# Kernel tuning notes

Hardware: AMD Instinct MI355X
Metric: run time of the kernel (lower is better)

## Reference

```python
import jax, jax.numpy as jnp
import numpy as np

B, H, W, CIN = 4, 32, 32, 3
COUT, NPAR = 4, 16

# Ansatz3x3 gate list: (control, target, base param index); each entry applies
# CRZ(theta[k], control, target) then CRX(theta[k+1], control, target).
GATES = [(1, 0, 0), (3, 2, 2), (2, 0, 4), (8, 7, 6),
         (5, 4, 8), (7, 6, 10), (6, 4, 12), (4, 0, 14)]
NQ = 9


def setup_inputs() -> dict:
    key = jax.random.key(0)
    k1, k2 = jax.random.split(key)
    x = jax.random.uniform(k1, (B, H, W, CIN), dtype=jnp.float32)
    q_params = jax.random.uniform(k2, (COUT, NPAR), minval=-np.pi, maxval=np.pi,
                                  dtype=jnp.float32)
    return {"x": x, "q_params": q_params}


def _rz_mat(th):
    # RZ(th) = diag(e^{-i th/2}, e^{+i th/2}); th: [C] -> [C,2,2]
    e = jnp.exp(-0.5j * th.astype(jnp.complex64))
    z = jnp.zeros_like(e)
    return jnp.stack([jnp.stack([e, z], -1), jnp.stack([z, jnp.conj(e)], -1)], -2)


def _rx_mat(th):
    # RX(th) = [[cos, -i sin], [-i sin, cos]] with half-angle; th: [C] -> [C,2,2]
    c = jnp.cos(0.5 * th).astype(jnp.complex64)
    s = (-1j * jnp.sin(0.5 * th)).astype(jnp.complex64)
    return jnp.stack([jnp.stack([c, s], -1), jnp.stack([s, c], -1)], -2)


def _apply_ctrl(state, U, control, target):
    # state: [C, P] + [2]*NQ (axis 2+q is qubit q); U: [C,2,2] applied on target
    # when control qubit is 1.
    ax_c, ax_t = 2 + control, 2 + target
    s0, s1 = jnp.split(state, 2, axis=ax_c)
    s1 = jnp.moveaxis(s1, ax_t, -1)
    s1 = jnp.einsum('cab,c...b->c...a', U, s1)
    s1 = jnp.moveaxis(s1, -1, ax_t)
    return jnp.concatenate([s0, s1], axis=ax_c)


def _quanv_forward(x, q_params):
    cout = q_params.shape[0]
    b, h, w = x.shape[0], x.shape[1], x.shape[2]
    fx, fy = h - 2, w - 2  # stride 1
    avg = jnp.mean(x, axis=-1)  # [B,H,W]
    # 3x3 patches, row-major flatten matching .flatten(): [B,fx,fy,9]
    patches = jnp.stack([avg[:, i:i + fx, j:j + fy]
                         for i in range(3) for j in range(3)], axis=-1)
    angles = 2.0 * jnp.pi * patches - jnp.pi
    # RX(angle)|0> = [cos(a/2), -i sin(a/2)] per qubit -> product state
    a0 = jnp.cos(0.5 * angles).astype(jnp.complex64)
    a1 = (-1j * jnp.sin(0.5 * angles)).astype(jnp.complex64)
    amps = jnp.stack([a0, a1], axis=-1).reshape(b * fx * fy, NQ, 2)  # [P,9,2]
    P = b * fx * fy
    state = amps[:, 0, :]  # [P,2]
    for q in range(1, NQ):
        state = state[..., None] * amps[:, q, :].reshape((P,) + (1,) * q + (2,))
    # replicate over output channels (params differ per channel)
    state = jnp.broadcast_to(state[None], (cout,) + state.shape) + 0j  # [C,P,2,...,2]
    for (ctrl, tgt, k) in GATES:
        state = _apply_ctrl(state, _rz_mat(q_params[:, k]), ctrl, tgt)
        state = _apply_ctrl(state, _rx_mat(q_params[:, k + 1]), ctrl, tgt)
    # avgZ = (p0 - p1 + 1)/2 = P(qubit0 = 0); qubit 0 is axis 2
    s = state[:, :, 0]  # [C,P] + [2]*8
    p0 = jnp.sum(s.real ** 2 + s.imag ** 2, axis=tuple(range(2, 2 + NQ - 1)))  # [C,P]
    out = jnp.zeros((b, h, w, cout), jnp.float32)
    vals = p0.reshape(cout, b, fx, fy).transpose(1, 2, 3, 0).astype(jnp.float32)
    return out.at[:, 1:1 + fx, 1:1 + fy, :].set(vals)


def reference(x, q_params):
    return _quanv_forward(x, q_params)
```

## Files before the change

kernel.cpp:

```cpp
#include <hip/hip_runtime.h>
#include <math.h>


namespace {
constexpr int kB = 4, kH = 32, kW = 32, kCIN = 3, kCOUT = 4;
constexpr int kFX = 30, kFY = 30;
constexpr float kPI = 3.14159265358979323846f;
}

template <int CTRL>
__device__ __forceinline__ float dpp_perm(float v) {
    return __int_as_float(
        __builtin_amdgcn_mov_dpp(__float_as_int(v), CTRL, 0xF, 0xF, true));
}
__device__ __forceinline__ float rdlane(float v, int l) {
    return __int_as_float(__builtin_amdgcn_readlane(__float_as_int(v), l));
}

#define CRZ_LR(CB, TBIT, K) do {                                           \
    const bool ctl = (lane & (CB)) != 0;                                   \
    const float ce = ctl ? gc[K] : 1.0f;                                   \
    const float se = ctl ? gs[K] : 0.0f;                                   \
    _Pragma("unroll")                                                      \
    for (int r = 0; r < 8; ++r) {                                          \
        const float sg = (r & (TBIT)) ? -se : se;                          \
        const float nr = ce * re[r] + sg * im[r];                          \
        const float ni = ce * im[r] - sg * re[r];                          \
        re[r] = nr; im[r] = ni;                                            \
    }                                                                      \
} while (0)

#define CRX_LR(CB, TBIT, K) do {                                           \
    const bool ctl = (lane & (CB)) != 0;                                   \
    const float ce = ctl ? gc[K] : 1.0f;                                   \
    const float se = ctl ? gs[K] : 0.0f;                                   \
    _Pragma("unroll")                                                      \
    for (int r = 0; r < 8; ++r) if (!(r & (TBIT))) {                       \
        const int r2 = r | (TBIT);                                         \
        const float ar = re[r], ai = im[r], br = re[r2], bi = im[r2];      \
        re[r]  = ce * ar - se * br;  im[r]  = ce * ai - se * bi;           \
        re[r2] = se * ar + ce * br;  im[r2] = se * ai + ce * bi;           \
    }                                                                      \
} while (0)

#define CRZ_RR(CBIT, TBIT, K) do {                                         \
    const float ce = gc[K], se = gs[K];                                    \
    _Pragma("unroll")                                                      \
    for (int r = 0; r < 8; ++r) if (r & (CBIT)) {                          \
        const float sg = (r & (TBIT)) ? -se : se;                          \
        const float nr = ce * re[r] + sg * im[r];                          \
        const float ni = ce * im[r] - sg * re[r];                          \
        re[r] = nr; im[r] = ni;                                            \
    }                                                                      \
} while (0)

#define CRX_RR(CBIT, TBIT, K) do {                                         \
    const float ce = gc[K], se = gs[K];                                    \
    _Pragma("unroll")                                                      \
    for (int r = 0; r < 8; ++r) if ((r & (CBIT)) && !(r & (TBIT))) {       \
        const int r2 = r | (TBIT);                                         \
        const float ar = re[r], ai = im[r], br = re[r2], bi = im[r2];      \
        re[r]  = ce * ar - se * br;  im[r]  = ce * ai - se * bi;           \
        re[r2] = se * ar + ce * br;  im[r2] = se * ai + ce * bi;           \
    }                                                                      \
} while (0)

#define CRZ_LL(CB, TB, K) do {                                             \
    const bool ctl = (lane & (CB)) != 0;                                   \
    const float ce  = ctl ? gc[K] : 1.0f;                                  \
    const float se0 = ctl ? gs[K] : 0.0f;                                  \
    const float se  = (lane & (TB)) ? -se0 : se0;                          \
    _Pragma("unroll")                                                      \
    for (int r = 0; r < 8; ++r) {                                          \
        const float nr = ce * re[r] + se * im[r];                          \
        const float ni = ce * im[r] - se * re[r];                          \
        re[r] = nr; im[r] = ni;                                            \
    }                                                                      \
} while (0)

#define CRX_LL_DPP(CB, TB, DPPC, K) do {                                   \
    const bool ctl = (lane & (CB)) != 0;                                   \
    const float ce  = ctl ? gc[K] : 1.0f;                                  \
    const float se0 = ctl ? gs[K] : 0.0f;                                  \
    const float se  = (lane & (TB)) ? se0 : -se0;                          \
    _Pragma("unroll")                                                      \
    for (int r = 0; r < 8; ++r) {                                          \
        const float pr  = dpp_perm<DPPC>(re[r]);                           \
        const float pim = dpp_perm<DPPC>(im[r]);                           \
        re[r] = ce * re[r] + se * pr;                                      \
        im[r] = ce * im[r] + se * pim;                                     \
    }                                                                      \
} while (0)

__global__ __launch_bounds__(256) void quanv9q_kernel(
    const float* __restrict__ x, const float* __restrict__ qp,
    float* __restrict__ out)
{
    const int lane = threadIdx.x & 63;
    const int wave = (blockIdx.x << 2) + (threadIdx.x >> 6);

    const int co  = wave & 3;
    const int p   = wave >> 2;
    const int b   = p / (kFX * kFY);
    const int rem = p - b * (kFX * kFY);
    const int oy  = rem / kFY;
    const int ox  = rem - oy * kFY;

    float myc = 0.f, mys = 0.f, mgc = 0.f, mgs = 0.f;
    if (lane < 9) {
        const int di = lane / 3, dj = lane - (lane / 3) * 3;
        const float* px = x + (((b * kH + (oy + di)) * kW + (ox + dj)) * kCIN);
        const float v = (px[0] + px[1] + px[2]) * (1.0f / 3.0f);
        sincosf(kPI * v - 0.5f * kPI, &mys, &myc);
    }
    if (lane < 16) {
        sincosf(0.5f * qp[co * 16 + lane], &mgs, &mgc);
    }
    float cq[9], sq[9];
    #pragma unroll
    for (int q = 0; q < 9; ++q) { cq[q] = __shfl(myc, q, 64); sq[q] = __shfl(mys, q, 64); }
    float gc[16], gs[16];
    #pragma unroll
    for (int k = 0; k < 16; ++k) { gc[k] = rdlane(mgc, k); gs[k] = rdlane(mgs, k); }

    float pm = 1.0f;
    pm *= (lane & 1)  ? sq[7] : cq[7];
    pm *= (lane & 2)  ? sq[6] : cq[6];
    pm *= (lane & 4)  ? sq[8] : cq[8];
    pm *= (lane & 8)  ? sq[5] : cq[5];
    pm *= (lane & 16) ? sq[3] : cq[3];
    pm *= (lane & 32) ? sq[1] : cq[1];

    float re[8], im[8];
    {
        const float a0 = pm * cq[0], a1 = pm * sq[0];
        const float b00 = a0 * cq[2], b01 = a0 * sq[2];
        const float b10 = a1 * cq[2], b11 = a1 * sq[2];
        re[0] = b00 * cq[4]; re[1] = b00 * sq[4];
        re[2] = b01 * cq[4]; re[3] = b01 * sq[4];
        re[4] = b10 * cq[4]; re[5] = b10 * sq[4];
        re[6] = b11 * cq[4]; re[7] = b11 * sq[4];
    }
    #pragma unroll
    for (int r = 0; r < 8; ++r) im[r] = 0.0f;

    CRZ_LR(32, 4, 0);   CRX_LR(32, 4, 1);
    CRZ_LR(16, 2, 2);   CRX_LR(16, 2, 3);
    CRZ_RR(2, 4, 4);    CRX_RR(2, 4, 5);
    CRZ_LL(4, 1, 6);    CRX_LL_DPP(4, 1, 0xB1, 7);
    CRZ_LR(8, 1, 8);    CRX_LR(8, 1, 9);
    CRZ_LL(1, 2, 10);   CRX_LL_DPP(1, 2, 0x4E, 11);
    CRZ_LR(2, 1, 12);   CRX_LR(2, 1, 13);
    CRZ_RR(1, 4, 14);   CRX_RR(1, 4, 15);

    float ssum = 0.0f;
    #pragma unroll
    for (int r = 0; r < 4; ++r) ssum += re[r] * re[r] + im[r] * im[r];
    #pragma unroll
    for (int off = 32; off > 0; off >>= 1) ssum += __shfl_xor(ssum, off, 64);

    if (lane == 0)
        out[((b * kH + (oy + 1)) * kW + (ox + 1)) * kCOUT + co] = ssum;
}

extern "C" void kernel_launch(void* const* d_in, const int* in_sizes, int n_in,
                              void* d_out, int out_size, void* d_ws, size_t ws_size,
                              hipStream_t stream) {
    const float* x  = (const float*)d_in[0];
    const float* qp = (const float*)d_in[1];
    float* out = (float*)d_out;

    hipMemsetAsync(d_out, 0, (size_t)out_size * sizeof(float), stream);

    const int total_waves = kB * kFX * kFY * kCOUT;
    const int threads = 256;
    const int blocks = total_waves * 64 / threads;
    quanv9q_kernel<<<blocks, threads, 0, stream>>>(x, qp, out);
}
```

Before: 73.80 us.

## Fold border zeroing into kernel and use hardware sin/cos instructions

Removes the separate hipMemsetAsync and has the kernel zero the border output elements itself, so there is one launch instead of two. It replaces sincosf with the v_sin_f32/v_cos_f32 instructions on angles pre-scaled to revolutions, which drops the range-reduction code but lowers accuracy. Cross-lane broadcasts switch from __shfl to readlane, and the first CRZ is specialised for the zero imaginary part. The border zeroing relies on the grid covering every output index.

```diff
diff --git a/kernel.cpp b/kernel.cpp
--- a/kernel.cpp
+++ b/kernel.cpp
@@ -5,7 +5,6 @@
 namespace {
 constexpr int kB = 4, kH = 32, kW = 32, kCIN = 3, kCOUT = 4;
 constexpr int kFX = 30, kFY = 30;
-constexpr float kPI = 3.14159265358979323846f;
 }
 
 template <int CTRL>
@@ -15,6 +14,12 @@
 }
 __device__ __forceinline__ float rdlane(float v, int l) {
     return __int_as_float(__builtin_amdgcn_readlane(__float_as_int(v), l));
+}
+__device__ __forceinline__ float sin_rev(float x) {
+    float r; asm("v_sin_f32 %0, %1" : "=v"(r) : "v"(x)); return r;
+}
+__device__ __forceinline__ float cos_rev(float x) {
+    float r; asm("v_cos_f32 %0, %1" : "=v"(r) : "v"(x)); return r;
 }
 
 #define CRZ_LR(CB, TBIT, K) do {                                           \
@@ -99,6 +104,14 @@
     const int lane = threadIdx.x & 63;
     const int wave = (blockIdx.x << 2) + (threadIdx.x >> 6);
 
+    {
+        const int t = (blockIdx.x << 8) + threadIdx.x;
+        if (t < kB * kH * kW * kCOUT) {
+            const int w = (t >> 2) & 31, h = (t >> 7) & 31;
+            if (h == 0 || h == 31 || w == 0 || w == 31) out[t] = 0.0f;
+        }
+    }
+
     const int co  = wave & 3;
     const int p   = wave >> 2;
     const int b   = p / (kFX * kFY);
@@ -106,19 +119,19 @@
     const int oy  = rem / kFY;
     const int ox  = rem - oy * kFY;
 
-    float myc = 0.f, mys = 0.f, mgc = 0.f, mgs = 0.f;
-    if (lane < 9) {
-        const int di = lane / 3, dj = lane - (lane / 3) * 3;
-        const float* px = x + (((b * kH + (oy + di)) * kW + (ox + dj)) * kCIN);
-        const float v = (px[0] + px[1] + px[2]) * (1.0f / 3.0f);
-        sincosf(kPI * v - 0.5f * kPI, &mys, &myc);
-    }
-    if (lane < 16) {
-        sincosf(0.5f * qp[co * 16 + lane], &mgs, &mgc);
-    }
+    const int li = lane < 9 ? lane : 0;
+    const int di = li / 3, dj = li - di * 3;
+    const float* px = x + (((b * kH + (oy + di)) * kW + (ox + dj)) * kCIN);
+    const float v = (px[0] + px[1] + px[2]) * (1.0f / 3.0f);
+    const float prev_ = 0.5f * v - 0.25f;
+    const float myc = cos_rev(prev_), mys = sin_rev(prev_);
+    const int gi = lane < 16 ? lane : 0;
+    const float ga = qp[co * 16 + gi] * 0.07957747154594767f;
+    const float mgc = cos_rev(ga), mgs = sin_rev(ga);
+
     float cq[9], sq[9];
     #pragma unroll
-    for (int q = 0; q < 9; ++q) { cq[q] = __shfl(myc, q, 64); sq[q] = __shfl(mys, q, 64); }
+    for (int q = 0; q < 9; ++q) { cq[q] = rdlane(myc, q); sq[q] = rdlane(mys, q); }
     float gc[16], gs[16];
     #pragma unroll
     for (int k = 0; k < 16; ++k) { gc[k] = rdlane(mgc, k); gs[k] = rdlane(mgs, k); }
@@ -141,10 +154,19 @@
         re[4] = b10 * cq[4]; re[5] = b10 * sq[4];
         re[6] = b11 * cq[4]; re[7] = b11 * sq[4];
     }
-    #pragma unroll
-    for (int r = 0; r < 8; ++r) im[r] = 0.0f;
 
-    CRZ_LR(32, 4, 0);   CRX_LR(32, 4, 1);
+    {
+        const bool ctl = (lane & 32) != 0;
+        const float ce = ctl ? gc[0] : 1.0f;
+        const float se = ctl ? gs[0] : 0.0f;
+        #pragma unroll
+        for (int r = 0; r < 8; ++r) {
+            const float sg = (r & 4) ? -se : se;
+            im[r] = -sg * re[r];
+            re[r] = ce * re[r];
+        }
+    }
+    CRX_LR(32, 4, 1);
     CRZ_LR(16, 2, 2);   CRX_LR(16, 2, 3);
     CRZ_RR(2, 4, 4);    CRX_RR(2, 4, 5);
     CRZ_LL(4, 1, 6);    CRX_LL_DPP(4, 1, 0xB1, 7);
@@ -170,8 +192,6 @@
     const float* qp = (const float*)d_in[1];
     float* out = (float*)d_out;
 
-    hipMemsetAsync(d_out, 0, (size_t)out_size * sizeof(float), stream);
-
     const int total_waves = kB * kFX * kFY * kCOUT;
     const int threads = 256;
     const int blocks = total_waves * 64 / threads;
```

After: 71.75 us. 2.8% less time.
